# Optimization experiments

Measured on AMD Instinct MI355X. Metric: run time of the kernel, lower is better.

Reference implementation:

```python
import math
import jax, jax.numpy as jnp
import numpy as np

B, N, DIM, H = 2, 4096, 1024, 16
DH = DIM // H
LEVELS = int(math.log2(N))
SCALE = 1.0 / math.sqrt(DH)


def build_lookup_table(seq_len):
    """Replicates build_hierarchical_index_lookup_table (numpy, static)."""
    levels = int(math.log2(seq_len))
    total_nodes = 2 * seq_len - 1
    max_valid = total_nodes - 2
    idx = np.full((seq_len, levels), -1, dtype=np.int32)
    cm = np.zeros((seq_len, levels), dtype=bool)
    for n in range(seq_len):
        nc = n
        for l in range(levels):
            if l == 0:
                pair = nc
                nn = nc ^ 1
            else:
                pair = nc // 2 + seq_len
                nn = pair ^ 1  # (nc//2 + seq_len) ^ 1 per Python precedence
            if nn > max_valid:
                break
            if pair < nn:
                cm[n, l] = True  # neighbor is to the right -> causally masked
            idx[n, l] = nn
            nc = nn
    return idx, cm


def setup_inputs() -> dict:
    key = jax.random.key(0)
    ks = jax.random.split(key, 12)
    w = lambda k: (jax.random.normal(k, (DIM, DIM), dtype=jnp.float32) * 0.02)
    idx_np, cm_np = build_lookup_table(N)
    return {
        "x": jax.random.normal(ks[0], (B, N, DIM), dtype=jnp.float32),
        "Wq_y": w(ks[1]), "Wk_y": w(ks[2]), "Wv_y": w(ks[3]),
        "Wo_y": w(ks[4]), "bo_y": jnp.zeros((DIM,), jnp.float32),
        "Wq_x": w(ks[5]), "Wk_x": w(ks[6]), "Wv_x": w(ks[7]),
        "Wo_x": w(ks[8]), "bo_x": jnp.zeros((DIM,), jnp.float32),
        "idx_map": jnp.asarray(idx_np, dtype=jnp.int32),       # [N, LEVELS]
        "causal_mask": jnp.asarray(cm_np, dtype=jnp.bool_),    # [N, LEVELS]
    }


def _heads(t):
    b, n, _ = t.shape
    return t.reshape(b, n, H, DH)


def _forward(x, Wq_y, Wk_y, Wv_y, Wo_y, bo_y, Wq_x, Wk_x, Wv_x, Wo_x, bo_x,
             idx_map, causal_mask):
    # ---- stage 1: build parent nodes level by level (online 2-child softmax merge)
    nodes = [x]  # leaves: [B, N, DIM]; parents appended level by level
    cur = x
    for _ in range(LEVELS):
        pre = 0.5 * (cur[:, 0::2] + cur[:, 1::2])     # parent query source [B,P,DIM]
        q = _heads(pre @ Wq_y)                        # [B,P,H,DH]
        k = _heads(cur @ Wk_y)                        # [B,C,H,DH]
        v = _heads(cur @ Wv_y)
        s0 = jnp.einsum('bphd,bphd->bph', q, k[:, 0::2]) * SCALE
        s1 = jnp.einsum('bphd,bphd->bph', q, k[:, 1::2]) * SCALE
        m = jnp.maximum(s0, s1)
        e0 = jnp.exp(s0 - m)
        e1 = jnp.exp(s1 - m)
        denom = e0 + e1 + 1e-9
        parent = ((e0 / denom)[..., None] * v[:, 0::2]
                  + (e1 / denom)[..., None] * v[:, 1::2])   # [B,P,H,DH]
        bp, pp = parent.shape[0], parent.shape[1]
        parent = parent.reshape(bp, pp, DIM) @ Wo_y + bo_y
        nodes.append(parent)
        cur = parent
    h_all = jnp.concatenate(nodes, axis=1)            # [B, 2N-1, DIM]

    # ---- stage 2: fused multi-level gather attention over self + neighbors
    Q = _heads(x @ Wq_x)                              # leaf queries [B,N,H,DH]
    K_all = _heads(h_all @ Wk_x)                      # [B,2N-1,H,DH]
    V_all = _heads(h_all @ Wv_x)

    k_cross = jnp.take(K_all, idx_map, axis=1)        # [B,N,LEVELS,H,DH]
    v_cross = jnp.take(V_all, idx_map, axis=1)

    s_self = jnp.einsum('bnhd,bnhd->bnh', Q, K_all[:, :N]) * SCALE   # [B,N,H]
    s_cross = jnp.einsum('bnhd,bnlhd->bnhl', Q, k_cross) * SCALE     # [B,N,H,L]
    neg_inf = jnp.float32(-jnp.inf)
    s_cross = jnp.where(causal_mask[None, :, None, :], neg_inf, s_cross)

    scores = jnp.concatenate([s_self[..., None], s_cross], axis=-1)  # [B,N,H,L+1]
    w = jax.nn.softmax(scores, axis=-1)
    out = (w[..., 0:1] * V_all[:, :N]
           + jnp.einsum('bnhl,bnlhd->bnhd', w[..., 1:], v_cross))    # [B,N,H,DH]
    return out.reshape(B, N, DIM) @ Wo_x + bo_x


def reference(x, Wq_y, Wk_y, Wv_y, Wo_y, bo_y, Wq_x, Wk_x, Wv_x, Wo_x, bo_x,
              idx_map, causal_mask):
    return _forward(x, Wq_y, Wk_y, Wv_y, Wo_y, bo_y,
                    Wq_x, Wk_x, Wv_x, Wo_x, bo_x, idx_map, causal_mask)
```

## Files before the change

kernel.cpp:

```cpp
#include <hip/hip_runtime.h>
#include <stdint.h>

#define H_NODES 8191
#define NN 4096
#define DIMC 1024

typedef __bf16 bf16x8 __attribute__((ext_vector_type(8)));
typedef float f32x4 __attribute__((ext_vector_type(4)));

__device__ __forceinline__ float b2f(ushort u) {
  union { uint32_t i; float f; } x; x.i = ((uint32_t)u) << 16; return x.f;
}
__device__ __forceinline__ ushort f2b(float f) {
  union { float f; uint32_t i; } x; x.f = f;
  uint32_t r = x.i + 0x7FFFu + ((x.i >> 16) & 1u);
  return (ushort)(r >> 16);
}
__device__ __forceinline__ void load16f(const ushort* p, float* f) {
  const uint32_t* w = (const uint32_t*)p;
  #pragma unroll
  for (int i = 0; i < 8; ++i) {
    uint32_t v = w[i];
    f[2 * i]     = b2f((ushort)(v & 0xffff));
    f[2 * i + 1] = b2f((ushort)(v >> 16));
  }
}
__device__ __forceinline__ void store16b(ushort* p, const float* f) {
  uint32_t w[8];
  #pragma unroll
  for (int i = 0; i < 8; ++i)
    w[i] = (uint32_t)f2b(f[2 * i]) | ((uint32_t)f2b(f[2 * i + 1]) << 16);
  *(uint4*)p = *(const uint4*)&w[0];
  *(uint4*)(p + 8) = *(const uint4*)&w[4];
}

struct WPtrs { const float* w[8]; };

__global__ void __launch_bounds__(256) transpose_w_k(WPtrs wp, ushort* __restrict__ dst) {
  __shared__ float t[32][33];
  const float* src = wp.w[blockIdx.z];
  int c0 = blockIdx.x * 32, r0 = blockIdx.y * 32;
  int tx = threadIdx.x, ty = threadIdx.y;
  #pragma unroll
  for (int i = ty; i < 32; i += 8)
    t[i][tx] = src[(long)(r0 + i) * DIMC + c0 + tx];
  __syncthreads();
  ushort* d = dst + (long)blockIdx.z * DIMC * DIMC;
  #pragma unroll
  for (int i = ty; i < 32; i += 8)
    d[(long)(c0 + i) * DIMC + r0 + tx] = f2b(t[tx][i]);
}

__global__ void __launch_bounds__(256) cvt_x_k(const float* __restrict__ x, ushort* __restrict__ h) {
  long t = (long)blockIdx.x * 256 + threadIdx.x;
  long i = t << 2;
  if (i >= (long)2 * NN * DIMC) return;
  long row = i >> 10;
  int col = (int)(i & 1023);
  long b = row >> 12;
  long n = row & 4095;
  float4 v = *(const float4*)(x + i);
  ushort* d = h + ((b * H_NODES + n) << 10) + col;
  uint2 pk;
  pk.x = (uint32_t)f2b(v.x) | ((uint32_t)f2b(v.y) << 16);
  pk.y = (uint32_t)f2b(v.z) | ((uint32_t)f2b(v.w) << 16);
  *(uint2*)d = pk;
}

__global__ void __launch_bounds__(256) avg_pairs_k(const ushort* __restrict__ h,
    ushort* __restrict__ pre, int P, int offL) {
  long t = (long)blockIdx.x * 256 + threadIdx.x;
  if (t >= (long)2 * P * 128) return;
  int dblk = (int)(t & 127);
  long r = t >> 7;
  int b = (r >= P) ? 1 : 0;
  int p = (int)(r - (long)b * P);
  const ushort* c = h + (((long)(b * H_NODES + offL + 2 * p)) << 10) + dblk * 8;
  const uint4 a0 = *(const uint4*)c;
  const uint4 a1 = *(const uint4*)(c + DIMC);
  const uint32_t* pa = (const uint32_t*)&a0;
  const uint32_t* pb = (const uint32_t*)&a1;
  uint32_t outw[4];
  #pragma unroll
  for (int i = 0; i < 4; ++i) {
    float x0 = b2f((ushort)(pa[i] & 0xffff)), x1 = b2f((ushort)(pa[i] >> 16));
    float y0 = b2f((ushort)(pb[i] & 0xffff)), y1 = b2f((ushort)(pb[i] >> 16));
    ushort r0 = f2b(0.5f * (x0 + y0)), r1 = f2b(0.5f * (x1 + y1));
    outw[i] = (uint32_t)r0 | ((uint32_t)r1 << 16);
  }
  *(uint4*)(pre + (((long)(b * P + p)) << 10) + dblk * 8) = *(const uint4*)outw;
}

struct GemmDesc {
  const ushort* A; long sAb;
  const ushort* Bt;
  const float* bias;
  void* C; long sCb; int ldc;
  int M; int outMode;
  int tX, tY;
};

__device__ __forceinline__ void stage_tile(const GemmDesc& d, const ushort* Ab,
    int row0, int col0, ushort* lA, ushort* lB, int kt, int wave, int lane) {
  #pragma unroll
  for (int j = 0; j < 2; ++j) {
    int s = wave * 128 + j * 64 + lane;
    int r = s >> 2;
    int g = (s & 3) ^ ((r >> 1) & 3);
    int gr = row0 + r; gr = (gr < d.M) ? gr : (d.M - 1);
    const ushort* srcA = Ab + (long)gr * DIMC + kt * 32 + g * 8;
    __builtin_amdgcn_global_load_lds(
        (const __attribute__((address_space(1))) void*)(uintptr_t)srcA,
        (__attribute__((address_space(3))) void*)(uint32_t)(uintptr_t)(lA + (wave * 128 + j * 64) * 8),
        16, 0, 0);
    const ushort* srcB = d.Bt + (long)(col0 + r) * DIMC + kt * 32 + g * 8;
    __builtin_amdgcn_global_load_lds(
        (const __attribute__((address_space(1))) void*)(uintptr_t)srcB,
        (__attribute__((address_space(3))) void*)(uint32_t)(uintptr_t)(lB + (wave * 128 + j * 64) * 8),
        16, 0, 0);
  }
}

__device__ void gemm_tile(const GemmDesc& d, int bz, int row0, int col0,
    ushort (*lA)[4096], ushort (*lB)[4096], int tid) {
  const ushort* Ab = d.A + (long)bz * d.sAb;
  int wave = tid >> 6, lane = tid & 63;
  int wr = wave >> 1, wc = wave & 1;

  f32x4 acc[4][4];
  #pragma unroll
  for (int m = 0; m < 4; ++m)
    #pragma unroll
    for (int n = 0; n < 4; ++n) acc[m][n] = (f32x4){0.f, 0.f, 0.f, 0.f};

  stage_tile(d, Ab, row0, col0, lA[0], lB[0], 0, wave, lane);
  stage_tile(d, Ab, row0, col0, lA[1], lB[1], 1, wave, lane);
  asm volatile("s_waitcnt vmcnt(4)" ::: "memory");
  __builtin_amdgcn_s_barrier();

  int rr = lane & 15, g4 = lane >> 4;
  for (int kt = 0; kt < 32; ++kt) {
    int cur = kt % 3;
    if (kt + 2 < 32)
      stage_tile(d, Ab, row0, col0, lA[(kt + 2) % 3], lB[(kt + 2) % 3], kt + 2, wave, lane);
    bf16x8 af[4], bfr[4];
    #pragma unroll
    for (int m = 0; m < 4; ++m) {
      int r = wr * 64 + m * 16 + rr;
      int slot = g4 ^ ((r >> 1) & 3);
      af[m] = *reinterpret_cast<const bf16x8*>(&lA[cur][r * 32 + slot * 8]);
    }
    #pragma unroll
    for (int n = 0; n < 4; ++n) {
      int r = wc * 64 + n * 16 + rr;
      int slot = g4 ^ ((r >> 1) & 3);
      bfr[n] = *reinterpret_cast<const bf16x8*>(&lB[cur][r * 32 + slot * 8]);
    }
    __builtin_amdgcn_s_setprio(1);
    #pragma unroll
    for (int m = 0; m < 4; ++m)
      #pragma unroll
      for (int n = 0; n < 4; ++n)
        acc[m][n] = __builtin_amdgcn_mfma_f32_16x16x32_bf16(af[m], bfr[n], acc[m][n], 0, 0, 0);
    __builtin_amdgcn_s_setprio(0);
    if (kt < 30) { asm volatile("s_waitcnt vmcnt(4)" ::: "memory"); }
    else         { asm volatile("s_waitcnt vmcnt(0)" ::: "memory"); }
    if (kt < 31) __builtin_amdgcn_s_barrier();
  }

  int rq = lane >> 4;
  #pragma unroll
  for (int n = 0; n < 4; ++n) {
    int col = col0 + wc * 64 + n * 16 + rr;
    float bv = d.bias ? d.bias[col] : 0.0f;
    #pragma unroll
    for (int m = 0; m < 4; ++m) {
      int gr0 = row0 + wr * 64 + m * 16 + rq * 4;
      #pragma unroll
      for (int r = 0; r < 4; ++r) {
        int gr = gr0 + r;
        if (gr < d.M) {
          float vv = acc[m][n][r] + bv;
          long o = (long)bz * d.sCb + (long)gr * d.ldc + col;
          if (d.outMode == 2) ((float*)d.C)[o] = vv;
          else ((ushort*)d.C)[o] = f2b(vv);
        }
      }
    }
  }
}

__global__ void __launch_bounds__(256) gemm_multi(GemmDesc d0, GemmDesc d1, int t0) {
  __shared__ __align__(16) ushort lA[3][4096];
  __shared__ __align__(16) ushort lB[3][4096];
  int t = blockIdx.x;
  const GemmDesc& d = (t < t0) ? d0 : d1;
  int u = (t < t0) ? t : t - t0;
  int per = d.tX * d.tY;
  int bz = u / per;
  int rem = u - bz * per;
  int ty = rem / d.tX;
  int tx = rem - ty * d.tX;
  gemm_tile(d, bz, tx * 128, ty * 128, lA, lB, threadIdx.x);
}

__global__ void __launch_bounds__(256) merge_y2_k(const ushort* __restrict__ q,
    const ushort* __restrict__ kv, ushort* __restrict__ outp, int P) {
  int wave = threadIdx.x >> 6, lane = threadIdx.x & 63;
  long w = (long)blockIdx.x * 4 + wave;
  if (w >= (long)2 * P) return;
  int b = (w >= P) ? 1 : 0;
  int p = (int)(w - (long)b * P);
  const ushort* qp = q + (((long)(b * P + p)) << 10) + lane * 16;
  const ushort* kvb = kv + ((long)(b * 2 * P + 2 * p)) * 2048;
  float qf[16], k0f[16], k1f[16];
  load16f(qp, qf);
  load16f(kvb + lane * 16, k0f);
  load16f(kvb + 2048 + lane * 16, k1f);
  float d0 = 0.f, d1 = 0.f;
  #pragma unroll
  for (int j = 0; j < 16; ++j) { d0 += qf[j] * k0f[j]; d1 += qf[j] * k1f[j]; }
  d0 += __shfl_xor(d0, 1); d0 += __shfl_xor(d0, 2);
  d1 += __shfl_xor(d1, 1); d1 += __shfl_xor(d1, 2);
  float s0 = d0 * 0.125f, s1 = d1 * 0.125f;
  float mm = fmaxf(s0, s1);
  float e0 = expf(s0 - mm), e1 = expf(s1 - mm);
  float inv = 1.0f / (e0 + e1 + 1e-9f);
  float w0 = e0 * inv, w1 = e1 * inv;
  float v0f[16], v1f[16], ov[16];
  load16f(kvb + 1024 + lane * 16, v0f);
  load16f(kvb + 2048 + 1024 + lane * 16, v1f);
  #pragma unroll
  for (int j = 0; j < 16; ++j) ov[j] = w0 * v0f[j] + w1 * v1f[j];
  store16b(outp + (((long)(b * P + p)) << 10) + lane * 16, ov);
}

__global__ void __launch_bounds__(256) attn_x2_k(const ushort* __restrict__ Q,
    const ushort* __restrict__ KV, ushort* __restrict__ outp) {
  int wave = threadIdx.x >> 6, lane = threadIdx.x & 63;
  long w = (long)blockIdx.x * 4 + wave;
  int n = (int)(w & 4095);
  int b = (int)(w >> 12);
  const ushort* KVb = KV + (long)b * H_NODES * 2048;
  float qf[16];
  load16f(Q + (((long)b * NN + n) << 10) + lane * 16, qf);
  int nb[13];
  nb[0] = n;
  #pragma unroll
  for (int l = 0; l < 12; ++l) nb[1 + l] = (8192 - (8192 >> l)) + ((n >> l) ^ 1);
  float s[13];
  #pragma unroll
  for (int i = 0; i < 13; ++i) {
    float kf[16];
    load16f(KVb + (long)nb[i] * 2048 + lane * 16, kf);
    float d = 0.f;
    #pragma unroll
    for (int j = 0; j < 16; ++j) d += qf[j] * kf[j];
    d += __shfl_xor(d, 1);
    d += __shfl_xor(d, 2);
    s[i] = d * 0.125f;
  }
  #pragma unroll
  for (int l = 0; l < 12; ++l)
    if (((n >> l) & 1) == 0) s[1 + l] = -__builtin_inff();
  float mm = s[0];
  #pragma unroll
  for (int i = 1; i < 13; ++i) mm = fmaxf(mm, s[i]);
  float e[13], sum = 0.f;
  #pragma unroll
  for (int i = 0; i < 13; ++i) { e[i] = expf(s[i] - mm); sum += e[i]; }
  float inv = 1.0f / sum;
  float ov[16];
  #pragma unroll
  for (int j = 0; j < 16; ++j) ov[j] = 0.f;
  #pragma unroll
  for (int i = 0; i < 13; ++i) {
    float wgt = e[i] * inv;
    float vf[16];
    load16f(KVb + (long)nb[i] * 2048 + 1024 + lane * 16, vf);
    #pragma unroll
    for (int j = 0; j < 16; ++j) ov[j] += wgt * vf[j];
  }
  store16b(outp + (((long)b * NN + n) << 10) + lane * 16, ov);
}

extern "C" void kernel_launch(void* const* d_in, const int* in_sizes, int n_in,
                              void* d_out, int out_size, void* d_ws, size_t ws_size,
                              hipStream_t stream) {
  const float* x    = (const float*)d_in[0];
  const float* Wq_y = (const float*)d_in[1];
  const float* Wk_y = (const float*)d_in[2];
  const float* Wv_y = (const float*)d_in[3];
  const float* Wo_y = (const float*)d_in[4];
  const float* bo_y = (const float*)d_in[5];
  const float* Wq_x = (const float*)d_in[6];
  const float* Wk_x = (const float*)d_in[7];
  const float* Wv_x = (const float*)d_in[8];
  const float* Wo_x = (const float*)d_in[9];
  const float* bo_x = (const float*)d_in[10];

  ushort* wt  = (ushort*)d_ws;
  ushort* h   = wt + (size_t)8 * 1024 * 1024;
  ushort* reg = h + (size_t)2 * H_NODES * DIMC;
  ushort* pre = reg;
  ushort* qb  = pre + (size_t)2 * 2048 * DIMC;
  ushort* kv1 = qb  + (size_t)2 * 2048 * DIMC;
  ushort* mrg = kv1 + (size_t)2 * 4096 * 2048;
  ushort* Qx   = reg;
  ushort* KVa  = Qx + (size_t)2 * 4096 * DIMC;
  ushort* aout = KVa + (size_t)2 * H_NODES * 2048;

  size_t need = ((size_t)8 * 1024 * 1024 + (size_t)2 * H_NODES * DIMC +
                 (size_t)2 * 4096 * DIMC + (size_t)2 * H_NODES * 2048 +
                 (size_t)2 * 4096 * DIMC) * 2;
  if (ws_size < need) return;

  WPtrs wp;
  wp.w[0] = Wq_y; wp.w[1] = Wk_y; wp.w[2] = Wv_y; wp.w[3] = Wo_y;
  wp.w[4] = Wq_x; wp.w[5] = Wk_x; wp.w[6] = Wv_x; wp.w[7] = Wo_x;
  transpose_w_k<<<dim3(32, 32, 8), dim3(32, 8), 0, stream>>>(wp, wt);
  cvt_x_k<<<8192, 256, 0, stream>>>(x, h);

  auto mkdesc = [](const ushort* A, long sAb, const ushort* Bt, const float* bias,
                   void* C, long sCb, int ldc, int M, int outMode, int tY) {
    GemmDesc d; d.A = A; d.sAb = sAb; d.Bt = Bt; d.bias = bias; d.C = C; d.sCb = sCb;
    d.ldc = ldc; d.M = M; d.outMode = outMode; d.tX = (M + 127) / 128; d.tY = tY;
    return d;
  };

  for (int l = 0; l < 12; ++l) {
    int C = NN >> l, P = C >> 1;
    int offL = 8192 - (8192 >> l);
    int offP = 8192 - (8192 >> (l + 1));
    avg_pairs_k<<<(2 * P * 128 + 255) / 256, 256, 0, stream>>>(h, pre, P, offL);
    GemmDesc dq = mkdesc(pre, (long)P * DIMC, wt, nullptr,
                         qb, (long)P * DIMC, DIMC, P, 0, 8);
    GemmDesc dkv = mkdesc(h + (long)offL * DIMC, (long)H_NODES * DIMC,
                          wt + (size_t)1 * 1024 * 1024, nullptr,
                          kv1, (long)C * 2048, 2048, C, 0, 16);
    int t0 = dq.tX * dq.tY * 2, t1 = dkv.tX * dkv.tY * 2;
    gemm_multi<<<t0 + t1, 256, 0, stream>>>(dq, dkv, t0);
    merge_y2_k<<<(2 * P + 3) / 4, 256, 0, stream>>>(qb, kv1, mrg, P);
    GemmDesc dgo = mkdesc(mrg, (long)P * DIMC, wt + (size_t)3 * 1024 * 1024, bo_y,
                          h + (long)offP * DIMC, (long)H_NODES * DIMC, DIMC, P, 1, 8);
    gemm_multi<<<dgo.tX * dgo.tY * 2, 256, 0, stream>>>(dgo, dgo, dgo.tX * dgo.tY * 2);
  }

  GemmDesc dqx = mkdesc(h, (long)H_NODES * DIMC, wt + (size_t)4 * 1024 * 1024, nullptr,
                        Qx, (long)4096 * DIMC, DIMC, 4096, 0, 8);
  GemmDesc dkva = mkdesc(h, (long)H_NODES * DIMC, wt + (size_t)5 * 1024 * 1024, nullptr,
                         KVa, (long)H_NODES * 2048, 2048, H_NODES, 0, 16);
  int t0 = dqx.tX * dqx.tY * 2, t1 = dkva.tX * dkva.tY * 2;
  gemm_multi<<<t0 + t1, 256, 0, stream>>>(dqx, dkva, t0);
  attn_x2_k<<<2048, 256, 0, stream>>>(Qx, KVa, aout);
  GemmDesc dox = mkdesc(aout, (long)4096 * DIMC, wt + (size_t)7 * 1024 * 1024, bo_x,
                        d_out, (long)4096 * DIMC, DIMC, 4096, 2, 8);
  gemm_multi<<<dox.tX * dox.tY * 2, 256, 0, stream>>>(dox, dox, dox.tX * dox.tY * 2);
}
```

Before: 784.4 us.

## Fuse pair averaging into Q projection, interleave final-stage GEMMs into tree levels

Removes the avg_pairs kernel by projecting children with Wq and averaging the projected queries inside the merge kernel, which relies on the linearity of the projection. K, V and Q for each level now come from one GEMM with 3072 output columns. The final-stage Qx and KV projections are split into slices and piggybacked onto the per-level GEMM launches as soon as those nodes exist, filling idle CUs on small levels. The GEMM pipeline also drops from triple to double LDS buffering with an extra barrier per k-step, which lowers LDS use but may expose more load latency.

```diff
diff --git a/kernel.cpp b/kernel.cpp
--- a/kernel.cpp
+++ b/kernel.cpp
@@ -65,30 +65,6 @@
   pk.x = (uint32_t)f2b(v.x) | ((uint32_t)f2b(v.y) << 16);
   pk.y = (uint32_t)f2b(v.z) | ((uint32_t)f2b(v.w) << 16);
   *(uint2*)d = pk;
-}
-
-__global__ void __launch_bounds__(256) avg_pairs_k(const ushort* __restrict__ h,
-    ushort* __restrict__ pre, int P, int offL) {
-  long t = (long)blockIdx.x * 256 + threadIdx.x;
-  if (t >= (long)2 * P * 128) return;
-  int dblk = (int)(t & 127);
-  long r = t >> 7;
-  int b = (r >= P) ? 1 : 0;
-  int p = (int)(r - (long)b * P);
-  const ushort* c = h + (((long)(b * H_NODES + offL + 2 * p)) << 10) + dblk * 8;
-  const uint4 a0 = *(const uint4*)c;
-  const uint4 a1 = *(const uint4*)(c + DIMC);
-  const uint32_t* pa = (const uint32_t*)&a0;
-  const uint32_t* pb = (const uint32_t*)&a1;
-  uint32_t outw[4];
-  #pragma unroll
-  for (int i = 0; i < 4; ++i) {
-    float x0 = b2f((ushort)(pa[i] & 0xffff)), x1 = b2f((ushort)(pa[i] >> 16));
-    float y0 = b2f((ushort)(pb[i] & 0xffff)), y1 = b2f((ushort)(pb[i] >> 16));
-    ushort r0 = f2b(0.5f * (x0 + y0)), r1 = f2b(0.5f * (x1 + y1));
-    outw[i] = (uint32_t)r0 | ((uint32_t)r1 << 16);
-  }
-  *(uint4*)(pre + (((long)(b * P + p)) << 10) + dblk * 8) = *(const uint4*)outw;
 }
 
 struct GemmDesc {
@@ -121,7 +97,7 @@
   }
 }
 
-__device__ void gemm_tile(const GemmDesc& d, int bz, int row0, int col0,
+__device__ __forceinline__ void gemm_tile(const GemmDesc& d, int bz, int row0, int col0,
     ushort (*lA)[4096], ushort (*lB)[4096], int tid) {
   const ushort* Ab = d.A + (long)bz * d.sAb;
   int wave = tid >> 6, lane = tid & 63;
@@ -134,15 +110,17 @@
     for (int n = 0; n < 4; ++n) acc[m][n] = (f32x4){0.f, 0.f, 0.f, 0.f};
 
   stage_tile(d, Ab, row0, col0, lA[0], lB[0], 0, wave, lane);
-  stage_tile(d, Ab, row0, col0, lA[1], lB[1], 1, wave, lane);
-  asm volatile("s_waitcnt vmcnt(4)" ::: "memory");
-  __builtin_amdgcn_s_barrier();
 
   int rr = lane & 15, g4 = lane >> 4;
   for (int kt = 0; kt < 32; ++kt) {
-    int cur = kt % 3;
-    if (kt + 2 < 32)
-      stage_tile(d, Ab, row0, col0, lA[(kt + 2) % 3], lB[(kt + 2) % 3], kt + 2, wave, lane);
+    int cur = kt & 1;
+    if (kt + 1 < 32) {
+      stage_tile(d, Ab, row0, col0, lA[cur ^ 1], lB[cur ^ 1], kt + 1, wave, lane);
+      asm volatile("s_waitcnt vmcnt(4)" ::: "memory");
+    } else {
+      asm volatile("s_waitcnt vmcnt(0)" ::: "memory");
+    }
+    __builtin_amdgcn_s_barrier();
     bf16x8 af[4], bfr[4];
     #pragma unroll
     for (int m = 0; m < 4; ++m) {
@@ -163,9 +141,7 @@
       for (int n = 0; n < 4; ++n)
         acc[m][n] = __builtin_amdgcn_mfma_f32_16x16x32_bf16(af[m], bfr[n], acc[m][n], 0, 0, 0);
     __builtin_amdgcn_s_setprio(0);
-    if (kt < 30) { asm volatile("s_waitcnt vmcnt(4)" ::: "memory"); }
-    else         { asm volatile("s_waitcnt vmcnt(0)" ::: "memory"); }
-    if (kt < 31) __builtin_amdgcn_s_barrier();
+    __builtin_amdgcn_s_barrier();
   }
 
   int rq = lane >> 4;
@@ -191,8 +167,8 @@
 }
 
 __global__ void __launch_bounds__(256) gemm_multi(GemmDesc d0, GemmDesc d1, int t0) {
-  __shared__ __align__(16) ushort lA[3][4096];
-  __shared__ __align__(16) ushort lB[3][4096];
+  __shared__ __align__(16) ushort lA[2][4096];
+  __shared__ __align__(16) ushort lB[2][4096];
   int t = blockIdx.x;
   const GemmDesc& d = (t < t0) ? d0 : d1;
   int u = (t < t0) ? t : t - t0;
@@ -204,22 +180,26 @@
   gemm_tile(d, bz, tx * 128, ty * 128, lA, lB, threadIdx.x);
 }
 
-__global__ void __launch_bounds__(256) merge_y2_k(const ushort* __restrict__ q,
-    const ushort* __restrict__ kv, ushort* __restrict__ outp, int P) {
+__global__ void __launch_bounds__(256) merge_y3_k(const ushort* __restrict__ kvq,
+    ushort* __restrict__ outp, int P) {
   int wave = threadIdx.x >> 6, lane = threadIdx.x & 63;
   long w = (long)blockIdx.x * 4 + wave;
   if (w >= (long)2 * P) return;
   int b = (w >= P) ? 1 : 0;
   int p = (int)(w - (long)b * P);
-  const ushort* qp = q + (((long)(b * P + p)) << 10) + lane * 16;
-  const ushort* kvb = kv + ((long)(b * 2 * P + 2 * p)) * 2048;
-  float qf[16], k0f[16], k1f[16];
-  load16f(qp, qf);
-  load16f(kvb + lane * 16, k0f);
-  load16f(kvb + 2048 + lane * 16, k1f);
+  const ushort* c0 = kvq + ((long)(b * 2 * P + 2 * p)) * 3072;
+  const ushort* c1 = c0 + 3072;
+  float q0[16], q1[16], k0f[16], k1f[16];
+  load16f(c0 + 2048 + lane * 16, q0);
+  load16f(c1 + 2048 + lane * 16, q1);
+  load16f(c0 + lane * 16, k0f);
+  load16f(c1 + lane * 16, k1f);
   float d0 = 0.f, d1 = 0.f;
   #pragma unroll
-  for (int j = 0; j < 16; ++j) { d0 += qf[j] * k0f[j]; d1 += qf[j] * k1f[j]; }
+  for (int j = 0; j < 16; ++j) {
+    float qv = 0.5f * (q0[j] + q1[j]);
+    d0 += qv * k0f[j]; d1 += qv * k1f[j];
+  }
   d0 += __shfl_xor(d0, 1); d0 += __shfl_xor(d0, 2);
   d1 += __shfl_xor(d1, 1); d1 += __shfl_xor(d1, 2);
   float s0 = d0 * 0.125f, s1 = d1 * 0.125f;
@@ -228,8 +208,8 @@
   float inv = 1.0f / (e0 + e1 + 1e-9f);
   float w0 = e0 * inv, w1 = e1 * inv;
   float v0f[16], v1f[16], ov[16];
-  load16f(kvb + 1024 + lane * 16, v0f);
-  load16f(kvb + 2048 + 1024 + lane * 16, v1f);
+  load16f(c0 + 1024 + lane * 16, v0f);
+  load16f(c1 + 1024 + lane * 16, v1f);
   #pragma unroll
   for (int j = 0; j < 16; ++j) ov[j] = w0 * v0f[j] + w1 * v1f[j];
   store16b(outp + (((long)(b * P + p)) << 10) + lane * 16, ov);
@@ -301,59 +281,80 @@
 
   ushort* wt  = (ushort*)d_ws;
   ushort* h   = wt + (size_t)8 * 1024 * 1024;
-  ushort* reg = h + (size_t)2 * H_NODES * DIMC;
-  ushort* pre = reg;
-  ushort* qb  = pre + (size_t)2 * 2048 * DIMC;
-  ushort* kv1 = qb  + (size_t)2 * 2048 * DIMC;
-  ushort* mrg = kv1 + (size_t)2 * 4096 * 2048;
-  ushort* Qx   = reg;
-  ushort* KVa  = Qx + (size_t)2 * 4096 * DIMC;
+  ushort* Qx  = h + (size_t)2 * H_NODES * DIMC;
+  ushort* KVa = Qx + (size_t)2 * 4096 * DIMC;
   ushort* aout = KVa + (size_t)2 * H_NODES * 2048;
-
-  size_t need = ((size_t)8 * 1024 * 1024 + (size_t)2 * H_NODES * DIMC +
-                 (size_t)2 * 4096 * DIMC + (size_t)2 * H_NODES * 2048 +
-                 (size_t)2 * 4096 * DIMC) * 2;
-  if (ws_size < need) return;
+  ushort* kvq = aout;
+  ushort* mrg = kvq + (size_t)2 * 4096 * 3072;
+
+  size_t wsElems = (size_t)8 * 1024 * 1024 + (size_t)2 * H_NODES * DIMC +
+                   (size_t)2 * 4096 * DIMC + (size_t)2 * H_NODES * 2048 +
+                   (size_t)2 * 4096 * 3072 + (size_t)2 * 2048 * DIMC;
+  if (ws_size < wsElems * 2) return;
 
   WPtrs wp;
-  wp.w[0] = Wq_y; wp.w[1] = Wk_y; wp.w[2] = Wv_y; wp.w[3] = Wo_y;
+  wp.w[0] = Wk_y; wp.w[1] = Wv_y; wp.w[2] = Wq_y; wp.w[3] = Wo_y;
   wp.w[4] = Wq_x; wp.w[5] = Wk_x; wp.w[6] = Wv_x; wp.w[7] = Wo_x;
   transpose_w_k<<<dim3(32, 32, 8), dim3(32, 8), 0, stream>>>(wp, wt);
   cvt_x_k<<<8192, 256, 0, stream>>>(x, h);
 
-  auto mkdesc = [](const ushort* A, long sAb, const ushort* Bt, const float* bias,
-                   void* C, long sCb, int ldc, int M, int outMode, int tY) {
+  auto mk128 = [](const ushort* A, long sAb, const ushort* Bt, const float* bias,
+                  void* C, long sCb, int ldc, int M, int outMode, int tY) {
     GemmDesc d; d.A = A; d.sAb = sAb; d.Bt = Bt; d.bias = bias; d.C = C; d.sCb = sCb;
     d.ldc = ldc; d.M = M; d.outMode = outMode; d.tX = (M + 127) / 128; d.tY = tY;
     return d;
   };
+  auto kvSub = [&](long start, int len) {
+    return mk128(h + start * DIMC, (long)H_NODES * DIMC, wt + (size_t)5 * 1024 * 1024,
+                 nullptr, KVa + start * 2048, (long)H_NODES * 2048, 2048, len, 0, 16);
+  };
+  auto qSub = [&](long start, int len) {
+    return mk128(h + start * DIMC, (long)H_NODES * DIMC, wt + (size_t)4 * 1024 * 1024,
+                 nullptr, Qx + start * DIMC, (long)4096 * DIMC, DIMC, len, 0, 8);
+  };
+  auto tiles = [](const GemmDesc& d) { return d.tX * d.tY * 2; };
 
   for (int l = 0; l < 12; ++l) {
-    int C = NN >> l, P = C >> 1;
+    int P = NN >> (l + 1);
+    int C = 2 * P;
     int offL = 8192 - (8192 >> l);
     int offP = 8192 - (8192 >> (l + 1));
-    avg_pairs_k<<<(2 * P * 128 + 255) / 256, 256, 0, stream>>>(h, pre, P, offL);
-    GemmDesc dq = mkdesc(pre, (long)P * DIMC, wt, nullptr,
-                         qb, (long)P * DIMC, DIMC, P, 0, 8);
-    GemmDesc dkv = mkdesc(h + (long)offL * DIMC, (long)H_NODES * DIMC,
-                          wt + (size_t)1 * 1024 * 1024, nullptr,
-                          kv1, (long)C * 2048, 2048, C, 0, 16);
-    int t0 = dq.tX * dq.tY * 2, t1 = dkv.tX * dkv.tY * 2;
-    gemm_multi<<<t0 + t1, 256, 0, stream>>>(dq, dkv, t0);
-    merge_y2_k<<<(2 * P + 3) / 4, 256, 0, stream>>>(qb, kv1, mrg, P);
-    GemmDesc dgo = mkdesc(mrg, (long)P * DIMC, wt + (size_t)3 * 1024 * 1024, bo_y,
-                          h + (long)offP * DIMC, (long)H_NODES * DIMC, DIMC, P, 1, 8);
-    gemm_multi<<<dgo.tX * dgo.tY * 2, 256, 0, stream>>>(dgo, dgo, dgo.tX * dgo.tY * 2);
-  }
-
-  GemmDesc dqx = mkdesc(h, (long)H_NODES * DIMC, wt + (size_t)4 * 1024 * 1024, nullptr,
-                        Qx, (long)4096 * DIMC, DIMC, 4096, 0, 8);
-  GemmDesc dkva = mkdesc(h, (long)H_NODES * DIMC, wt + (size_t)5 * 1024 * 1024, nullptr,
-                         KVa, (long)H_NODES * 2048, 2048, H_NODES, 0, 16);
-  int t0 = dqx.tX * dqx.tY * 2, t1 = dkva.tX * dkva.tY * 2;
-  gemm_multi<<<t0 + t1, 256, 0, stream>>>(dqx, dkva, t0);
+
+    GemmDesc dkvq = mk128(h + (long)offL * DIMC, (long)H_NODES * DIMC, wt, nullptr,
+                          kvq, (long)C * 3072, 3072, C, 0, 24);
+    GemmDesc aK = dkvq; int nK = 0;
+    if      (l == 0) { aK = qSub(0, 4096);     nK = tiles(aK); }
+    else if (l == 1) { aK = kvSub(2048, 2048); nK = tiles(aK); }
+    else if (l == 2) { aK = kvSub(6144, 512);  nK = tiles(aK); }
+    else if (l == 3) { aK = kvSub(7168, 256);  nK = tiles(aK); }
+    else if (l == 4) { aK = kvSub(7680, 128);  nK = tiles(aK); }
+    else if (l == 5) { aK = kvSub(7936, 128);  nK = tiles(aK); }
+    int n0 = tiles(dkvq);
+    gemm_multi<<<n0 + nK, 256, 0, stream>>>(dkvq, aK, n0);
+
+    merge_y3_k<<<(2 * P + 3) / 4, 256, 0, stream>>>(kvq, mrg, P);
+
+    GemmDesc dgo = mk128(mrg, (long)P * DIMC, wt + (size_t)3 * 1024 * 1024, bo_y,
+                         h + (long)offP * DIMC, (long)H_NODES * DIMC, DIMC, P, 1, 8);
+    GemmDesc aO = dgo; int nO = 0;
+    if      (l == 0) { aO = kvSub(0, 2048);    nO = tiles(aO); }
+    else if (l == 1) { aO = kvSub(4096, 2048); nO = tiles(aO); }
+    else if (l == 2) { aO = kvSub(6656, 512);  nO = tiles(aO); }
+    else if (l == 3) { aO = kvSub(7424, 256);  nO = tiles(aO); }
+    else if (l == 4) { aO = kvSub(7808, 128);  nO = tiles(aO); }
+    int m0 = tiles(dgo);
+    gemm_multi<<<m0 + nO, 256, 0, stream>>>(dgo, aO, m0);
+  }
+
+  {
+    GemmDesc a0 = kvSub(8064, 127);
+    int n = tiles(a0);
+    gemm_multi<<<n, 256, 0, stream>>>(a0, a0, n);
+  }
   attn_x2_k<<<2048, 256, 0, stream>>>(Qx, KVa, aout);
-  GemmDesc dox = mkdesc(aout, (long)4096 * DIMC, wt + (size_t)7 * 1024 * 1024, bo_x,
-                        d_out, (long)4096 * DIMC, DIMC, 4096, 2, 8);
-  gemm_multi<<<dox.tX * dox.tY * 2, 256, 0, stream>>>(dox, dox, dox.tX * dox.tY * 2);
-}
+  {
+    GemmDesc dox = mk128(aout, (long)4096 * DIMC, wt + (size_t)7 * 1024 * 1024, bo_x,
+                         d_out, (long)4096 * DIMC, DIMC, 4096, 2, 8);
+    gemm_multi<<<tiles(dox), 256, 0, stream>>>(dox, dox, tiles(dox));
+  }
+}
```

Result: slower. 831.7 us (+6.0%).
